# Kernel tuning notes

Hardware: AMD Instinct MI355X
Metric: run time of the kernel (lower is better)

The kernel has to match this reference:

```python
import jax, jax.numpy as jnp
import numpy as np

# SectorAttention (PARTNER): dim=256, resolution=(4,4096), H_sp=4, W_sp=1, H=4, heads=8
B, Hq, Hres, Wres, C, NH = 4, 4, 4, 4096, 256, 8
H_SP, W_SP = 4, 1
HD = C // NH
SCALE = HD ** -0.5


def _forward(s, x, s_pos, x_pos, Wq, bq, Wk, bk, Wv, bv, Wo, bo,
             pw1, pb1, bn_g, bn_b, bn_m, bn_v, pw2, pb2,
             ln_g, ln_b, mw1, mb1, mw2, mb2):
    Bb, Lq, Cc = s.shape
    W = Wres
    nW = Bb * (W // W_SP)
    # ---- dynamic relative-position bias (per-window small conv net) ----
    xp = x_pos.reshape(Bb, Hq // H_SP, H_SP, W // W_SP, W_SP, 2)
    xp = jnp.transpose(xp, (0, 1, 3, 5, 2, 4)).reshape(-1, 2, H_SP * W_SP)   # (nW,2,4)
    sp = jnp.transpose(s_pos, (0, 2, 3, 1)).reshape(-1, 2, Hq * W_SP)        # (nW,2,4)
    rel = sp[:, :, :, None] - xp[:, :, None, :]                              # (nW,2,4,4)
    rel = rel.reshape(nW, 2, -1)                                             # (nW,2,16)
    h = jnp.einsum('oc,bcl->bol', pw1, rel) + pb1[None, :, None]             # Conv1d k=1
    h = (h - bn_m[None, :, None]) * jax.lax.rsqrt(bn_v[None, :, None] + 1e-5) \
        * bn_g[None, :, None] + bn_b[None, :, None]                          # BatchNorm1d (eval)
    h = jax.nn.relu(h)
    h = jnp.einsum('oc,bcl->bol', pw2, h) + pb2[None, :, None]               # Conv1d k=1 -> heads
    rel_bias = h.reshape(-1, NH, Hq, H_SP)                                   # (nW,NH,4,4) since W_SP==1
    # ---- projections + window partitioning ----
    q = s @ Wq.T + bq
    q = q.reshape(Bb, Cc, Hq, W)                          # faithful torch .view reinterpretation
    q = q.reshape(Bb, NH, HD, Hq, W // W_SP, W_SP)
    q = jnp.transpose(q, (0, 4, 1, 3, 5, 2)).reshape(-1, NH, Hq * W_SP, HD)

    def im2cswin(t):
        t = jnp.transpose(t, (0, 2, 1)).reshape(Bb, Cc, Hres, W)
        t = t.reshape(Bb, Cc, Hres // H_SP, H_SP, W // W_SP, W_SP)
        t = jnp.transpose(t, (0, 2, 4, 3, 5, 1)).reshape(-1, H_SP * W_SP, Cc)
        return jnp.transpose(t.reshape(-1, H_SP * W_SP, NH, HD), (0, 2, 1, 3))

    k = im2cswin(x @ Wk.T + bk)
    v = im2cswin(x @ Wv.T + bv)
    # ---- windowed attention with dynamic bias ----
    attn = jnp.einsum('wnqd,wnkd->wnqk', q * SCALE, k) + rel_bias
    attn = jax.nn.softmax(attn, axis=-1)
    o = jnp.einsum('wnqk,wnkd->wnqd', attn, v)            # (nW,NH,4,HD)
    o = jnp.transpose(o, (0, 2, 1, 3)).reshape(-1, Hq * W_SP, Cc)
    # windows2img(o, H_sp=Hq, W_sp=W_SP, H=Hq, W=W)
    o = o.reshape(Bb, Hq // Hq, W // W_SP, Hq, W_SP, Cc)
    o = jnp.transpose(o, (0, 1, 3, 2, 4, 5)).reshape(Bb, Hq * W, Cc)
    o = o @ Wo.T + bo
    s1 = s + o
    # ---- LayerNorm + MLP (residual) ----
    mu = jnp.mean(s1, axis=-1, keepdims=True)
    var = jnp.mean((s1 - mu) ** 2, axis=-1, keepdims=True)
    n = (s1 - mu) * jax.lax.rsqrt(var + 1e-5) * ln_g + ln_b
    h2 = jax.nn.gelu(n @ mw1.T + mb1, approximate=False)
    return s1 + h2 @ mw2.T + mb2


def setup_inputs() -> dict:
    key = jax.random.key(0)
    ks = jax.random.split(key, 12)
    rn = lambda k, sh, sc=1.0: jax.random.normal(k, sh, dtype=jnp.float32) * sc
    H4 = 4 * C
    return {
        's': rn(ks[0], (B, Hq * Wres, C)),
        'x': rn(ks[1], (B, Hres * Wres, C)),
        's_pos': rn(ks[2], (B, 2, Wres // W_SP, Hq * W_SP)),
        'x_pos': rn(ks[3], (B, Hres * Wres, 2)),
        'Wq': rn(ks[4], (C, C), 0.02), 'bq': jnp.zeros((C,), jnp.float32),
        'Wk': rn(ks[5], (C, C), 0.02), 'bk': jnp.zeros((C,), jnp.float32),
        'Wv': rn(ks[6], (C, C), 0.02), 'bv': jnp.zeros((C,), jnp.float32),
        'Wo': rn(ks[7], (C, C), 0.02), 'bo': jnp.zeros((C,), jnp.float32),
        'pw1': rn(ks[8], (16, 2), 0.2), 'pb1': jnp.zeros((16,), jnp.float32),
        'bn_g': jnp.ones((16,), jnp.float32), 'bn_b': jnp.zeros((16,), jnp.float32),
        'bn_m': jnp.zeros((16,), jnp.float32), 'bn_v': jnp.ones((16,), jnp.float32),
        'pw2': rn(ks[9], (NH, 16), 0.2), 'pb2': jnp.zeros((NH,), jnp.float32),
        'ln_g': jnp.ones((C,), jnp.float32), 'ln_b': jnp.zeros((C,), jnp.float32),
        'mw1': rn(ks[10], (H4, C), 0.02), 'mb1': jnp.zeros((H4,), jnp.float32),
        'mw2': rn(ks[11], (C, H4), 0.02), 'mb2': jnp.zeros((C,), jnp.float32),
    }


def reference(s, x, s_pos, x_pos, Wq, bq, Wk, bk, Wv, bv, Wo, bo,
              pw1, pb1, bn_g, bn_b, bn_m, bn_v, pw2, pb2,
              ln_g, ln_b, mw1, mb1, mw2, mb2):
    return _forward(s, x, s_pos, x_pos, Wq, bq, Wk, bk, Wv, bv, Wo, bo,
                    pw1, pb1, bn_g, bn_b, bn_m, bn_v, pw2, pb2,
                    ln_g, ln_b, mw1, mb1, mw2, mb2)
```

## Files before the change

### kernel.cpp

```cpp
#include <hip/hip_runtime.h>
#include <hip/hip_bf16.h>
#include <math.h>

typedef __hip_bfloat16 BF;
typedef __bf16 bf16x8 __attribute__((ext_vector_type(8)));
typedef float f32x4 __attribute__((ext_vector_type(4)));

struct alignas(8) BF4 { BF v[4]; };
struct alignas(16) BF8 { BF v[8]; };

static __device__ __forceinline__ float b2f(BF x) { return __bfloat162float(x); }
static __device__ __forceinline__ BF f2b(float x) { return __float2bfloat16(x); }

static __device__ __forceinline__ void gld_lds16(const void* g, void* l) {
  __builtin_amdgcn_global_load_lds(
      (const __attribute__((address_space(1))) unsigned int*)g,
      (__attribute__((address_space(3))) unsigned int*)l, 16, 0, 0);
}

__global__ void __launch_bounds__(256) cvt_kernel(
    const float* __restrict__ in, BF* __restrict__ out, int n4) {
  for (int i = blockIdx.x * 256 + threadIdx.x; i < n4; i += gridDim.x * 256) {
    float4 v = ((const float4*)in)[i];
    BF4 o;
    o.v[0] = f2b(v.x); o.v[1] = f2b(v.y); o.v[2] = f2b(v.z); o.v[3] = f2b(v.w);
    ((BF4*)out)[i] = o;
  }
}

__global__ void __launch_bounds__(256) bkv_kernel(
    const float* __restrict__ bk, const float* __restrict__ bv,
    float* __restrict__ bkv) {
  int i = blockIdx.x * 256 + threadIdx.x;
  bkv[i] = (i < 256) ? bk[i] : bv[i - 256];
}

__global__ void __launch_bounds__(256) bias_kernel(
    const float* __restrict__ s_pos, const float* __restrict__ x_pos,
    const float* __restrict__ pw1, const float* __restrict__ pb1,
    const float* __restrict__ bn_g, const float* __restrict__ bn_b,
    const float* __restrict__ bn_m, const float* __restrict__ bn_v,
    const float* __restrict__ pw2, const float* __restrict__ pb2,
    float* __restrict__ out) {
  int gid = blockIdx.x * 256 + threadIdx.x;
  int w = gid >> 4, l = gid & 15;
  int b = w >> 12, wi = w & 4095;
  int i = l >> 2, j = l & 3;
  int e0 = i, e1 = 4 + i;
  float sp0 = s_pos[(((size_t)b * 2 + (e0 & 1)) * 4096 + wi) * 4 + (e0 >> 1)];
  float sp1 = s_pos[(((size_t)b * 2 + (e1 & 1)) * 4096 + wi) * 4 + (e1 >> 1)];
  float xp0 = x_pos[((size_t)b * 16384 + j * 4096 + wi) * 2 + 0];
  float xp1 = x_pos[((size_t)b * 16384 + j * 4096 + wi) * 2 + 1];
  float r0 = sp0 - xp0, r1 = sp1 - xp1;
  float acc[8];
#pragma unroll
  for (int p = 0; p < 8; ++p) acc[p] = pb2[p];
#pragma unroll
  for (int o = 0; o < 16; ++o) {
    float t = pw1[o * 2 + 0] * r0 + pw1[o * 2 + 1] * r1 + pb1[o];
    float sc = bn_g[o] / sqrtf(bn_v[o] + 1e-5f);
    t = (t - bn_m[o]) * sc + bn_b[o];
    t = fmaxf(t, 0.0f);
#pragma unroll
    for (int p = 0; p < 8; ++p) acc[p] += pw2[p * 16 + o] * t;
  }
#pragma unroll
  for (int p = 0; p < 8; ++p) out[(size_t)w * 128 + p * 16 + l] = acc[p];
}

enum { EPI_NONE = 0, EPI_RES = 1, EPI_GELU = 2 };

template <int EPI, typename AT, typename RT, typename CT>
__global__ void __launch_bounds__(256, 2) gemm_tn(
    const AT* __restrict__ A, const BF* __restrict__ Bw,
    const float* __restrict__ bias, const RT* __restrict__ Res,
    CT* __restrict__ C, int M, int N, int K) {
  constexpr bool F32A = __is_same(AT, float);
  alignas(16) __shared__ BF As[8][128][8];
  alignas(16) __shared__ BF Bs[8][128][8];
  const int ntiles = N >> 7;
  const int cpx = gridDim.x >> 3;
  const int bid = blockIdx.x;
  const int swz = (bid & 7) * cpx + (bid >> 3);
  const int mt = swz / ntiles, nt = swz % ntiles;
  const int row0 = mt << 7, col0 = nt << 7;
  const int t = threadIdx.x;
  const int wave = t >> 6, lane = t & 63;
  const int wr = wave >> 1, wc = wave & 1;
  const int sm = t & 127;
  const int skc = t >> 7;
  f32x4 acc[4][4] = {};
  const int NT = K >> 6;
  float4 ar[4][2];

  auto stageB = [&](int kt) {
#pragma unroll
    for (int i = 0; i < 4; ++i) {
      const int kc = i * 2 + skc;
      gld_lds16(Bw + (size_t)(col0 + sm) * K + kt * 64 + kc * 8,
                &Bs[0][0][0] + (size_t)(i * 256 + wave * 64) * 8);
    }
  };
  auto loadA = [&](int kt) {
    if constexpr (F32A) {
#pragma unroll
      for (int i = 0; i < 4; ++i) {
        const int kc = i * 2 + skc;
        const float* src = A + (size_t)(row0 + sm) * K + kt * 64 + kc * 8;
        ar[i][0] = ((const float4*)src)[0];
        ar[i][1] = ((const float4*)src)[1];
      }
    }
  };
  auto writeA = [&]() {
    if constexpr (F32A) {
#pragma unroll
      for (int i = 0; i < 4; ++i) {
        const int kc = i * 2 + skc;
        BF tmp[8];
        tmp[0] = f2b(ar[i][0].x); tmp[1] = f2b(ar[i][0].y);
        tmp[2] = f2b(ar[i][0].z); tmp[3] = f2b(ar[i][0].w);
        tmp[4] = f2b(ar[i][1].x); tmp[5] = f2b(ar[i][1].y);
        tmp[6] = f2b(ar[i][1].z); tmp[7] = f2b(ar[i][1].w);
        *(bf16x8*)(&As[kc][sm][0]) = *(bf16x8*)tmp;
      }
    }
  };
  auto stageA_bf = [&](int kt) {
    if constexpr (!F32A) {
#pragma unroll
      for (int i = 0; i < 4; ++i) {
        const int kc = i * 2 + skc;
        gld_lds16((const BF*)A + (size_t)(row0 + sm) * K + kt * 64 + kc * 8,
                  &As[0][0][0] + (size_t)(i * 256 + wave * 64) * 8);
      }
    }
  };
  auto compute = [&]() {
#pragma unroll
    for (int kk = 0; kk < 2; ++kk) {
      const int chunk = kk * 4 + (lane >> 4);
      const int rl = lane & 15;
      bf16x8 af[4], bfr[4];
#pragma unroll
      for (int mi = 0; mi < 4; ++mi)
        af[mi] = *(const bf16x8*)(&As[chunk][wr * 64 + mi * 16 + rl][0]);
#pragma unroll
      for (int ni = 0; ni < 4; ++ni)
        bfr[ni] = *(const bf16x8*)(&Bs[chunk][wc * 64 + ni * 16 + rl][0]);
#pragma unroll
      for (int mi = 0; mi < 4; ++mi)
#pragma unroll
        for (int ni = 0; ni < 4; ++ni)
          acc[mi][ni] = __builtin_amdgcn_mfma_f32_16x16x32_bf16(
              af[mi], bfr[ni], acc[mi][ni], 0, 0, 0);
    }
  };

  loadA(0);
  for (int kt = 0; kt < NT; ++kt) {
    writeA();
    stageA_bf(kt);
    stageB(kt);
    if (kt + 1 < NT) loadA(kt + 1);
    __syncthreads();
    compute();
    __syncthreads();
  }

  const int rl = lane & 15, rg = lane >> 4;
#pragma unroll
  for (int mi = 0; mi < 4; ++mi) {
#pragma unroll
    for (int ni = 0; ni < 4; ++ni) {
      const int col = col0 + wc * 64 + ni * 16 + rl;
      const float bcol = bias[col];
#pragma unroll
      for (int r = 0; r < 4; ++r) {
        const int row = row0 + wr * 64 + mi * 16 + rg * 4 + r;
        float v = acc[mi][ni][r] + bcol;
        if constexpr (EPI == EPI_GELU)
          v = 0.5f * v * (1.0f + erff(v * 0.70710678118654752f));
        if constexpr (EPI == EPI_RES) {
          if constexpr (__is_same(RT, float))
            v += Res[(size_t)row * N + col];
          else
            v += b2f(Res[(size_t)row * N + col]);
        }
        if constexpr (__is_same(CT, float))
          C[(size_t)row * N + col] = v;
        else
          C[(size_t)row * N + col] = f2b(v);
      }
    }
  }
}

__global__ void __launch_bounds__(256, 2) gemm_q(
    const float* __restrict__ A, const BF* __restrict__ Bw,
    const float* __restrict__ bias, BF* __restrict__ Qa) {
  constexpr int K = 256;
  alignas(16) __shared__ BF As[8][128][8];
  alignas(16) __shared__ BF Bs[8][128][8];
  const int cpx = gridDim.x >> 3;
  const int bid = blockIdx.x;
  const int swz = (bid & 7) * cpx + (bid >> 3);
  const int mt = swz >> 1, nt = swz & 1;
  const int hp = mt & 3, qi = (mt >> 2) & 3, nh = (mt >> 4) & 7, bb = mt >> 7;
  const int col0 = nt << 7;
  const int t = threadIdx.x;
  const int wave = t >> 6, lane = t & 63;
  const int wr = wave >> 1, wc = wave & 1;
  const int sm = t & 127;
  const int skc = t >> 7;
  const size_t grow = (size_t)bb * 16384 + nh * 2048 + (size_t)(sm & 31) * 64 +
                      qi * 16 + hp * 4 + (sm >> 5);
  f32x4 acc[4][4] = {};
  float4 ar[4][2];

  auto stageB = [&](int kt) {
#pragma unroll
    for (int i = 0; i < 4; ++i) {
      const int kc = i * 2 + skc;
      gld_lds16(Bw + (size_t)(col0 + sm) * K + kt * 64 + kc * 8,
                &Bs[0][0][0] + (size_t)(i * 256 + wave * 64) * 8);
    }
  };
  auto loadA = [&](int kt) {
#pragma unroll
    for (int i = 0; i < 4; ++i) {
      const int kc = i * 2 + skc;
      const float* src = A + grow * K + kt * 64 + kc * 8;
      ar[i][0] = ((const float4*)src)[0];
      ar[i][1] = ((const float4*)src)[1];
    }
  };
  auto writeA = [&]() {
#pragma unroll
    for (int i = 0; i < 4; ++i) {
      const int kc = i * 2 + skc;
      BF tmp[8];
      tmp[0] = f2b(ar[i][0].x); tmp[1] = f2b(ar[i][0].y);
      tmp[2] = f2b(ar[i][0].z); tmp[3] = f2b(ar[i][0].w);
      tmp[4] = f2b(ar[i][1].x); tmp[5] = f2b(ar[i][1].y);
      tmp[6] = f2b(ar[i][1].z); tmp[7] = f2b(ar[i][1].w);
      *(bf16x8*)(&As[kc][sm][0]) = *(bf16x8*)tmp;
    }
  };
  auto compute = [&]() {
#pragma unroll
    for (int kk = 0; kk < 2; ++kk) {
      const int chunk = kk * 4 + (lane >> 4);
      const int rl = lane & 15;
      bf16x8 af[4], bfr[4];
#pragma unroll
      for (int mi = 0; mi < 4; ++mi)
        af[mi] = *(const bf16x8*)(&As[chunk][wr * 64 + mi * 16 + rl][0]);
#pragma unroll
      for (int ni = 0; ni < 4; ++ni)
        bfr[ni] = *(const bf16x8*)(&Bs[chunk][wc * 64 + ni * 16 + rl][0]);
#pragma unroll
      for (int mi = 0; mi < 4; ++mi)
#pragma unroll
        for (int ni = 0; ni < 4; ++ni)
          acc[mi][ni] = __builtin_amdgcn_mfma_f32_16x16x32_bf16(
              af[mi], bfr[ni], acc[mi][ni], 0, 0, 0);
    }
  };

  loadA(0);
  for (int kt = 0; kt < 4; ++kt) {
    writeA();
    stageB(kt);
    if (kt + 1 < 4) loadA(kt + 1);
    __syncthreads();
    compute();
    __syncthreads();
  }

  const int rl = lane & 15, rg = lane >> 4;
  const float SCALE = 0.17677669529663689f;
#pragma unroll
  for (int mi = 0; mi < 4; ++mi) {
#pragma unroll
    for (int ni = 0; ni < 4; ++ni) {
      const int col = col0 + wc * 64 + ni * 16 + rl;
      const float bcol = bias[col];
      const int i0 = wr * 64 + mi * 16 + rg * 4;
      const int hd = i0 & 31, hil = i0 >> 5;
      const int wi = (hp * 4 + hil) * 256 + col;
      BF4 pk;
#pragma unroll
      for (int r = 0; r < 4; ++r)
        pk.v[r] = f2b((acc[mi][ni][r] + bcol) * SCALE);
      *(BF4*)(Qa + ((((size_t)bb * 4096 + wi) * 8 + nh) * 128 + qi * 32 + hd)) = pk;
    }
  }
}

__global__ void __launch_bounds__(256) attn_kernel(
    const BF* __restrict__ Qa, const BF* __restrict__ KV,
    const float* __restrict__ biasb, BF* __restrict__ O) {
  const int t = threadIdx.x;
  const int g = t >> 4, l16 = t & 15;
  const int qi = l16 >> 2, kj = l16 & 3;
  const int w = (blockIdx.x << 1) | (g >> 3);
  const int nh = g & 7;
  const int b = w >> 12, wi = w & 4095;

  const uint4* qp = (const uint4*)(Qa + ((((size_t)b * 4096 + wi) * 8 + nh) * 128 + qi * 32));
  uint4 qv[4] = {qp[0], qp[1], qp[2], qp[3]};
  const uint4* kp = (const uint4*)(KV + ((size_t)b * 16384 + kj * 4096 + wi) * 512 + nh * 32);
  uint4 kv[4] = {kp[0], kp[1], kp[2], kp[3]};
  const float bias_l = biasb[(size_t)w * 128 + nh * 16 + l16];
  const BF* vbase = KV + (size_t)b * 16384 * 512 + 256 + nh * 32 + kj * 8;
  uint4 vv[4];
#pragma unroll
  for (int d = 0; d < 4; ++d)
    vv[d] = *(const uint4*)(vbase + ((size_t)((kj ^ d) * 4096 + wi)) * 512);

  float accs[4] = {0.f, 0.f, 0.f, 0.f};
#pragma unroll
  for (int j = 0; j < 4; ++j) {
#pragma unroll
    for (int e = 0; e < 4; ++e) {
      unsigned qe = ((const unsigned*)&qv[j])[e];
      unsigned ke = ((const unsigned*)&kv[j])[e];
      float ql = __uint_as_float(qe << 16);
      float qh = __uint_as_float(qe & 0xffff0000u);
      float kl = __uint_as_float(ke << 16);
      float kh = __uint_as_float(ke & 0xffff0000u);
      accs[e] = fmaf(ql, kl, accs[e]);
      accs[e] = fmaf(qh, kh, accs[e]);
    }
  }
  const float score = accs[0] + accs[1] + accs[2] + accs[3] + bias_l;

  float mx = fmaxf(score, __shfl_xor(score, 1));
  mx = fmaxf(mx, __shfl_xor(mx, 2));
  float e = __expf(score - mx);
  float sm = e + __shfl_xor(e, 1);
  sm += __shfl_xor(sm, 2);
  float p = e / sm;
  float pd[4];
  pd[0] = p;
  pd[1] = __shfl_xor(p, 1);
  pd[2] = __shfl_xor(p, 2);
  pd[3] = __shfl_xor(pd[1], 2);

  float o8[8] = {0.f, 0.f, 0.f, 0.f, 0.f, 0.f, 0.f, 0.f};
#pragma unroll
  for (int d = 0; d < 4; ++d) {
#pragma unroll
    for (int e2 = 0; e2 < 4; ++e2) {
      unsigned ve = ((const unsigned*)&vv[d])[e2];
      o8[e2 * 2 + 0] = fmaf(pd[d], __uint_as_float(ve << 16), o8[e2 * 2 + 0]);
      o8[e2 * 2 + 1] = fmaf(pd[d], __uint_as_float(ve & 0xffff0000u), o8[e2 * 2 + 1]);
    }
  }
  BF8 ob;
#pragma unroll
  for (int h = 0; h < 8; ++h) ob.v[h] = f2b(o8[h]);
  *(BF8*)(O + ((size_t)b * 16384 + qi * 4096 + wi) * 256 + nh * 32 + kj * 8) = ob;
}

__global__ void __launch_bounds__(256) ln_kernel(
    const BF* __restrict__ S1, const float* __restrict__ g,
    const float* __restrict__ be, BF* __restrict__ Nout) {
  const int wave = threadIdx.x >> 6, lane = threadIdx.x & 63;
  const size_t row = (size_t)blockIdx.x * 4 + wave;
  BF4 d = *(const BF4*)(S1 + row * 256 + lane * 4);
  float x[4] = {b2f(d.v[0]), b2f(d.v[1]), b2f(d.v[2]), b2f(d.v[3])};
  float s = x[0] + x[1] + x[2] + x[3];
  float sq = x[0] * x[0] + x[1] * x[1] + x[2] * x[2] + x[3] * x[3];
#pragma unroll
  for (int m = 1; m <= 32; m <<= 1) {
    s += __shfl_xor(s, m);
    sq += __shfl_xor(sq, m);
  }
  const float mean = s * 0.00390625f;
  const float var = sq * 0.00390625f - mean * mean;
  const float rstd = 1.0f / sqrtf(var + 1e-5f);
  BF4 o;
#pragma unroll
  for (int jj = 0; jj < 4; ++jj) {
    float nv = (x[jj] - mean) * rstd * g[lane * 4 + jj] + be[lane * 4 + jj];
    o.v[jj] = f2b(nv);
  }
  *(BF4*)(Nout + row * 256 + lane * 4) = o;
}

extern "C" void kernel_launch(void* const* d_in, const int* in_sizes, int n_in,
                              void* d_out, int out_size, void* d_ws, size_t ws_size,
                              hipStream_t stream) {
  const float* s     = (const float*)d_in[0];
  const float* x     = (const float*)d_in[1];
  const float* s_pos = (const float*)d_in[2];
  const float* x_pos = (const float*)d_in[3];
  const float* Wq = (const float*)d_in[4];  const float* bq = (const float*)d_in[5];
  const float* Wk = (const float*)d_in[6];  const float* bk = (const float*)d_in[7];
  const float* Wv = (const float*)d_in[8];  const float* bv = (const float*)d_in[9];
  const float* Wo = (const float*)d_in[10]; const float* bo = (const float*)d_in[11];
  const float* pw1 = (const float*)d_in[12]; const float* pb1 = (const float*)d_in[13];
  const float* bn_g = (const float*)d_in[14]; const float* bn_b = (const float*)d_in[15];
  const float* bn_m = (const float*)d_in[16]; const float* bn_v = (const float*)d_in[17];
  const float* pw2 = (const float*)d_in[18]; const float* pb2 = (const float*)d_in[19];
  const float* ln_g = (const float*)d_in[20]; const float* ln_b = (const float*)d_in[21];
  const float* mw1 = (const float*)d_in[22]; const float* mb1 = (const float*)d_in[23];
  const float* mw2 = (const float*)d_in[24]; const float* mb2 = (const float*)d_in[25];

  char* ws = (char*)d_ws;
  float* biasb = (float*)ws;
  BF* Qa   = (BF*)(ws + 8388608);
  BF* KVw  = (BF*)(ws + 41943040);
  BF* S1   = (BF*)(ws + 109051904);
  BF* Wq_bf  = (BF*)(ws + 142606336);
  BF* Wo_bf  = (BF*)(ws + 142737408);
  BF* Wkv_bf = (BF*)(ws + 142868480);
  BF* mw1_bf = (BF*)(ws + 143130624);
  BF* mw2_bf = (BF*)(ws + 143654912);
  float* bkv = (float*)(ws + 144179200);
  BF* Nw = Qa;
  BF* H2 = KVw;
  BF* ObBF = (BF*)d_out;
  float* Of = (float*)d_out;

  cvt_kernel<<<64, 256, 0, stream>>>(Wq, Wq_bf, 16384);
  cvt_kernel<<<64, 256, 0, stream>>>(Wo, Wo_bf, 16384);
  cvt_kernel<<<64, 256, 0, stream>>>(Wk, Wkv_bf, 16384);
  cvt_kernel<<<64, 256, 0, stream>>>(Wv, Wkv_bf + 65536, 16384);
  cvt_kernel<<<256, 256, 0, stream>>>(mw1, mw1_bf, 65536);
  cvt_kernel<<<256, 256, 0, stream>>>(mw2, mw2_bf, 65536);
  bkv_kernel<<<2, 256, 0, stream>>>(bk, bv, bkv);
  bias_kernel<<<1024, 256, 0, stream>>>(s_pos, x_pos, pw1, pb1, bn_g, bn_b,
                                        bn_m, bn_v, pw2, pb2, biasb);

  gemm_q<<<1024, 256, 0, stream>>>(s, Wq_bf, bq, Qa);
  gemm_tn<EPI_NONE, float, float, BF><<<2048, 256, 0, stream>>>(
      x, Wkv_bf, bkv, nullptr, KVw, 65536, 512, 256);
  attn_kernel<<<8192, 256, 0, stream>>>(Qa, KVw, biasb, ObBF);
  gemm_tn<EPI_RES, BF, float, BF><<<1024, 256, 0, stream>>>(
      ObBF, Wo_bf, bo, s, S1, 65536, 256, 256);
  ln_kernel<<<16384, 256, 0, stream>>>(S1, ln_g, ln_b, Nw);
  for (int h = 0; h < 2; ++h) {
    const size_t ro = (size_t)h * 32768;
    gemm_tn<EPI_GELU, BF, float, BF><<<2048, 256, 0, stream>>>(
        Nw + ro * 256, mw1_bf, mb1, nullptr, H2, 32768, 1024, 256);
    gemm_tn<EPI_RES, BF, BF, float><<<512, 256, 0, stream>>>(
        H2, mw2_bf, mb2, S1 + ro * 256, Of + ro * 256, 32768, 256, 1024);
  }
}
```

Baseline: 401.2 us.

## Double-buffer LDS tiles in GEMM kernels with explicit vmcnt waits

Both GEMM kernels now keep two LDS buffers for A and B tiles. The next K-tile's global-to-LDS loads (and the fp32 A register loads) are issued before computing on the current tile, and partial s_waitcnt vmcnt counts let loads for tile k+1 stay in flight during the MFMA work on tile k. This is meant to hide global memory latency behind compute. In exchange it doubles shared memory use per block, which may lower occupancy, and it depends on hand-counted vmcnt values matching the order in which the compiler issues loads.

```diff
diff --git a/kernel.cpp b/kernel.cpp
--- a/kernel.cpp
+++ b/kernel.cpp
@@ -76,8 +76,8 @@
     const float* __restrict__ bias, const RT* __restrict__ Res,
     CT* __restrict__ C, int M, int N, int K) {
   constexpr bool F32A = __is_same(AT, float);
-  alignas(16) __shared__ BF As[8][128][8];
-  alignas(16) __shared__ BF Bs[8][128][8];
+  alignas(16) __shared__ BF As[2][8][128][8];
+  alignas(16) __shared__ BF Bs[2][8][128][8];
   const int ntiles = N >> 7;
   const int cpx = gridDim.x >> 3;
   const int bid = blockIdx.x;
@@ -93,12 +93,12 @@
   const int NT = K >> 6;
   float4 ar[4][2];
 
-  auto stageB = [&](int kt) {
+  auto stageB = [&](int kt, int d) {
 #pragma unroll
     for (int i = 0; i < 4; ++i) {
       const int kc = i * 2 + skc;
       gld_lds16(Bw + (size_t)(col0 + sm) * K + kt * 64 + kc * 8,
-                &Bs[0][0][0] + (size_t)(i * 256 + wave * 64) * 8);
+                &Bs[d][0][0][0] + (size_t)(i * 256 + wave * 64) * 8);
     }
   };
   auto loadA = [&](int kt) {
@@ -112,7 +112,7 @@
       }
     }
   };
-  auto writeA = [&]() {
+  auto writeA = [&](int d) {
     if constexpr (F32A) {
 #pragma unroll
       for (int i = 0; i < 4; ++i) {
@@ -122,21 +122,21 @@
         tmp[2] = f2b(ar[i][0].z); tmp[3] = f2b(ar[i][0].w);
         tmp[4] = f2b(ar[i][1].x); tmp[5] = f2b(ar[i][1].y);
         tmp[6] = f2b(ar[i][1].z); tmp[7] = f2b(ar[i][1].w);
-        *(bf16x8*)(&As[kc][sm][0]) = *(bf16x8*)tmp;
-      }
-    }
-  };
-  auto stageA_bf = [&](int kt) {
+        *(bf16x8*)(&As[d][kc][sm][0]) = *(bf16x8*)tmp;
+      }
+    }
+  };
+  auto stageA_bf = [&](int kt, int d) {
     if constexpr (!F32A) {
 #pragma unroll
       for (int i = 0; i < 4; ++i) {
         const int kc = i * 2 + skc;
         gld_lds16((const BF*)A + (size_t)(row0 + sm) * K + kt * 64 + kc * 8,
-                  &As[0][0][0] + (size_t)(i * 256 + wave * 64) * 8);
-      }
-    }
-  };
-  auto compute = [&]() {
+                  &As[d][0][0][0] + (size_t)(i * 256 + wave * 64) * 8);
+      }
+    }
+  };
+  auto compute = [&](int d) {
 #pragma unroll
     for (int kk = 0; kk < 2; ++kk) {
       const int chunk = kk * 4 + (lane >> 4);
@@ -144,10 +144,10 @@
       bf16x8 af[4], bfr[4];
 #pragma unroll
       for (int mi = 0; mi < 4; ++mi)
-        af[mi] = *(const bf16x8*)(&As[chunk][wr * 64 + mi * 16 + rl][0]);
+        af[mi] = *(const bf16x8*)(&As[d][chunk][wr * 64 + mi * 16 + rl][0]);
 #pragma unroll
       for (int ni = 0; ni < 4; ++ni)
-        bfr[ni] = *(const bf16x8*)(&Bs[chunk][wc * 64 + ni * 16 + rl][0]);
+        bfr[ni] = *(const bf16x8*)(&Bs[d][chunk][wc * 64 + ni * 16 + rl][0]);
 #pragma unroll
       for (int mi = 0; mi < 4; ++mi)
 #pragma unroll
@@ -157,15 +157,38 @@
     }
   };
 
-  loadA(0);
+  if constexpr (F32A) {
+    stageB(0, 0);
+    loadA(0);
+  } else {
+    stageA_bf(0, 0);
+    stageB(0, 0);
+  }
   for (int kt = 0; kt < NT; ++kt) {
-    writeA();
-    stageA_bf(kt);
-    stageB(kt);
-    if (kt + 1 < NT) loadA(kt + 1);
-    __syncthreads();
-    compute();
-    __syncthreads();
+    const int cur = kt & 1, nxt = cur ^ 1;
+    const bool more = kt + 1 < NT;
+    if constexpr (F32A) {
+      writeA(cur);
+      if (more) {
+        stageB(kt + 1, nxt);
+        loadA(kt + 1);
+        asm volatile("s_waitcnt vmcnt(12) lgkmcnt(0)" ::: "memory");
+      } else {
+        asm volatile("s_waitcnt vmcnt(0) lgkmcnt(0)" ::: "memory");
+      }
+    } else {
+      if (more) {
+        stageA_bf(kt + 1, nxt);
+        stageB(kt + 1, nxt);
+        asm volatile("s_waitcnt vmcnt(8)" ::: "memory");
+      } else {
+        asm volatile("s_waitcnt vmcnt(0)" ::: "memory");
+      }
+    }
+    __builtin_amdgcn_s_barrier();
+    __builtin_amdgcn_sched_barrier(0);
+    compute(cur);
+    __builtin_amdgcn_s_barrier();
   }
 
   const int rl = lane & 15, rg = lane >> 4;
@@ -200,8 +223,8 @@
     const float* __restrict__ A, const BF* __restrict__ Bw,
     const float* __restrict__ bias, BF* __restrict__ Qa) {
   constexpr int K = 256;
-  alignas(16) __shared__ BF As[8][128][8];
-  alignas(16) __shared__ BF Bs[8][128][8];
+  alignas(16) __shared__ BF As[2][8][128][8];
+  alignas(16) __shared__ BF Bs[2][8][128][8];
   const int cpx = gridDim.x >> 3;
   const int bid = blockIdx.x;
   const int swz = (bid & 7) * cpx + (bid >> 3);
@@ -218,12 +241,12 @@
   f32x4 acc[4][4] = {};
   float4 ar[4][2];
 
-  auto stageB = [&](int kt) {
+  auto stageB = [&](int kt, int d) {
 #pragma unroll
     for (int i = 0; i < 4; ++i) {
       const int kc = i * 2 + skc;
       gld_lds16(Bw + (size_t)(col0 + sm) * K + kt * 64 + kc * 8,
-                &Bs[0][0][0] + (size_t)(i * 256 + wave * 64) * 8);
+                &Bs[d][0][0][0] + (size_t)(i * 256 + wave * 64) * 8);
     }
   };
   auto loadA = [&](int kt) {
@@ -235,7 +258,7 @@
       ar[i][1] = ((const float4*)src)[1];
     }
   };
-  auto writeA = [&]() {
+  auto writeA = [&](int d) {
 #pragma unroll
     for (int i = 0; i < 4; ++i) {
       const int kc = i * 2 + skc;
@@ -244,10 +267,10 @@
       tmp[2] = f2b(ar[i][0].z); tmp[3] = f2b(ar[i][0].w);
       tmp[4] = f2b(ar[i][1].x); tmp[5] = f2b(ar[i][1].y);
       tmp[6] = f2b(ar[i][1].z); tmp[7] = f2b(ar[i][1].w);
-      *(bf16x8*)(&As[kc][sm][0]) = *(bf16x8*)tmp;
-    }
-  };
-  auto compute = [&]() {
+      *(bf16x8*)(&As[d][kc][sm][0]) = *(bf16x8*)tmp;
+    }
+  };
+  auto compute = [&](int d) {
 #pragma unroll
     for (int kk = 0; kk < 2; ++kk) {
       const int chunk = kk * 4 + (lane >> 4);
@@ -255,10 +278,10 @@
       bf16x8 af[4], bfr[4];
 #pragma unroll
       for (int mi = 0; mi < 4; ++mi)
-        af[mi] = *(const bf16x8*)(&As[chunk][wr * 64 + mi * 16 + rl][0]);
+        af[mi] = *(const bf16x8*)(&As[d][chunk][wr * 64 + mi * 16 + rl][0]);
 #pragma unroll
       for (int ni = 0; ni < 4; ++ni)
-        bfr[ni] = *(const bf16x8*)(&Bs[chunk][wc * 64 + ni * 16 + rl][0]);
+        bfr[ni] = *(const bf16x8*)(&Bs[d][chunk][wc * 64 + ni * 16 + rl][0]);
 #pragma unroll
       for (int mi = 0; mi < 4; ++mi)
 #pragma unroll
@@ -268,14 +291,23 @@
     }
   };
 
+  stageB(0, 0);
   loadA(0);
   for (int kt = 0; kt < 4; ++kt) {
-    writeA();
-    stageB(kt);
-    if (kt + 1 < 4) loadA(kt + 1);
-    __syncthreads();
-    compute();
-    __syncthreads();
+    const int cur = kt & 1, nxt = cur ^ 1;
+    const bool more = kt + 1 < 4;
+    writeA(cur);
+    if (more) {
+      stageB(kt + 1, nxt);
+      loadA(kt + 1);
+      asm volatile("s_waitcnt vmcnt(12) lgkmcnt(0)" ::: "memory");
+    } else {
+      asm volatile("s_waitcnt vmcnt(0) lgkmcnt(0)" ::: "memory");
+    }
+    __builtin_amdgcn_s_barrier();
+    __builtin_amdgcn_sched_barrier(0);
+    compute(cur);
+    __builtin_amdgcn_s_barrier();
   }
 
   const int rl = lane & 15, rg = lane >> 4;
```

New measurement: 435.3 us. +8.5%, slower.
